# Performance work log

Measured on AMD Instinct MI355X. Metric: run time of the kernel, lower is better.

Reference implementation:

```python
import jax, jax.numpy as jnp
import numpy as np

N_L = 1600   # sample_number_l
N_R = 64     # sample_number_r
F = 512      # num_rgbxyz_feature


def setup_inputs() -> dict:
    key = jax.random.key(0)
    ks = jax.random.split(key, 6)
    soutput_l = jax.random.normal(ks[0], (200000, F), dtype=jnp.float32)
    soutput_r = jax.random.normal(ks[1], (100000, F), dtype=jnp.float32)
    W1 = jax.random.normal(ks[2], (2 * F, 512), dtype=jnp.float32) * 0.02
    b1 = jnp.zeros((512,), dtype=jnp.float32)
    W2 = jax.random.normal(ks[3], (512, 2), dtype=jnp.float32) * 0.02
    b2 = jnp.zeros((2,), dtype=jnp.float32)
    sample_idx_l = jax.random.randint(ks[4], (N_L,), 0, 200000)
    sample_idx_r = jax.random.randint(ks[5], (N_R,), 0, 100000)
    return {
        'soutput_l': soutput_l, 'soutput_r': soutput_r,
        'W1': W1, 'b1': b1, 'W2': W2, 'b2': b2,
        'sample_idx_l': sample_idx_l, 'sample_idx_r': sample_idx_r,
    }


def reference(soutput_l, soutput_r, W1, b1, W2, b2, sample_idx_l, sample_idx_r):
    # Gather sampled per-point features (replaces torch.randint sampling)
    fl = soutput_l[sample_idx_l]          # [N_l, F]
    fr = soutput_r[sample_idx_r]          # [N_r, F]
    n_l, feat = fl.shape
    n_r = fr.shape[0]
    # All-pairs concat: equivalent to the python loop over the 64 right samples,
    # each doing cat((feat_l, feat_r[i].repeat(N_l,1)), dim=1)
    cat = jnp.concatenate([
        jnp.broadcast_to(fl[:, None, :], (n_l, n_r, feat)),
        jnp.broadcast_to(fr[None, :, :], (n_l, n_r, feat)),
    ], axis=-1)                            # [N_l, N_r, 2F]
    # base3DPoseNet: 2-layer MLP (no batch norm), logits over 2 classes
    h = jax.nn.relu(jnp.einsum('lrf,fh->lrh', cat, W1) + b1)   # [N_l, N_r, 512]
    logits = jnp.einsum('lrh,hc->lrc', h, W2) + b2             # [N_l, N_r, 2]
    # softmax over class dim, take P(match) -> correspondence_map[N_l, N_r]
    correspondence_map = jax.nn.softmax(logits, axis=-1)[..., 1]
    return correspondence_map
```

## Files before the change

### kernel.cpp

```cpp
#include <hip/hip_runtime.h>
#include <math.h>

#define FDIM 512
#define NL 1600
#define NR 64

typedef __attribute__((ext_vector_type(8))) short short8;
typedef __attribute__((ext_vector_type(4))) float f32x4;
typedef __attribute__((ext_vector_type(4))) int   int4v;

__device__ __forceinline__ int cvtpk(float lo, float hi) {
    int r;
    asm("v_cvt_pk_bf16_f32 %0, %1, %2" : "=v"(r) : "v"(lo), "v"(hi));
    return r;
}

__global__ __launch_bounds__(64) void k_gemm(
    const float* __restrict__ SL, const float* __restrict__ SR,
    const float* __restrict__ W1, const float* __restrict__ b1,
    const int* __restrict__ idxL, const int* __restrict__ idxR,
    float* __restrict__ A, float* __restrict__ Bm)
{
    const int bm = blockIdx.x;
    const int bn = blockIdx.y;
    const bool isB = bm >= 50;
    const int n0 = bn * 32;
    const int lane = threadIdx.x, row = lane & 15, g = lane >> 4;

    const float* a0p; const float* a1p;
    if (isB) {
        const int rb = (bm - 50) * 32;
        a0p = SR + (long)idxR[rb + row] * FDIM;
        a1p = SR + (long)idxR[rb + 16 + row] * FDIM;
    } else {
        const int mb = bm * 32;
        a0p = SL + (long)idxL[mb + row] * FDIM;
        a1p = SL + (long)idxL[mb + 16 + row] * FDIM;
    }
    const float* w0 = W1 + (isB ? (long)FDIM * FDIM : 0) + (n0 + row);
    const float* w1 = w0 + 16;

    f32x4 acc00 = {}, acc01 = {}, acc10 = {}, acc11 = {};
    float4 a0r[2][2], a1r[2][2];
    float  b0r[2][8], b1r[2][8];

    {
        a0r[0][0] = *(const float4*)(a0p + g * 8);
        a0r[0][1] = *(const float4*)(a0p + g * 8 + 4);
        a1r[0][0] = *(const float4*)(a1p + g * 8);
        a1r[0][1] = *(const float4*)(a1p + g * 8 + 4);
        #pragma unroll
        for (int jj = 0; jj < 8; ++jj) {
            b0r[0][jj] = w0[(long)(g * 8 + jj) * FDIM];
            b1r[0][jj] = w1[(long)(g * 8 + jj) * FDIM];
        }
    }

    #pragma unroll
    for (int kk = 0; kk < 16; ++kk) {
        const int cur = kk & 1, nxt = cur ^ 1;
        if (kk < 15) {
            const int kb = (kk + 1) * 32 + g * 8;
            a0r[nxt][0] = *(const float4*)(a0p + kb);
            a0r[nxt][1] = *(const float4*)(a0p + kb + 4);
            a1r[nxt][0] = *(const float4*)(a1p + kb);
            a1r[nxt][1] = *(const float4*)(a1p + kb + 4);
            #pragma unroll
            for (int jj = 0; jj < 8; ++jj) {
                b0r[nxt][jj] = w0[(long)(kb + jj) * FDIM];
                b1r[nxt][jj] = w1[(long)(kb + jj) * FDIM];
            }
        }
        int4v a0, a1, b0, b1;
        a0.x = cvtpk(a0r[cur][0].x, a0r[cur][0].y);
        a0.y = cvtpk(a0r[cur][0].z, a0r[cur][0].w);
        a0.z = cvtpk(a0r[cur][1].x, a0r[cur][1].y);
        a0.w = cvtpk(a0r[cur][1].z, a0r[cur][1].w);
        a1.x = cvtpk(a1r[cur][0].x, a1r[cur][0].y);
        a1.y = cvtpk(a1r[cur][0].z, a1r[cur][0].w);
        a1.z = cvtpk(a1r[cur][1].x, a1r[cur][1].y);
        a1.w = cvtpk(a1r[cur][1].z, a1r[cur][1].w);
        b0.x = cvtpk(b0r[cur][0], b0r[cur][1]);
        b0.y = cvtpk(b0r[cur][2], b0r[cur][3]);
        b0.z = cvtpk(b0r[cur][4], b0r[cur][5]);
        b0.w = cvtpk(b0r[cur][6], b0r[cur][7]);
        b1.x = cvtpk(b1r[cur][0], b1r[cur][1]);
        b1.y = cvtpk(b1r[cur][2], b1r[cur][3]);
        b1.z = cvtpk(b1r[cur][4], b1r[cur][5]);
        b1.w = cvtpk(b1r[cur][6], b1r[cur][7]);
        const short8 A0 = *(const short8*)&a0, A1 = *(const short8*)&a1;
        const short8 B0 = *(const short8*)&b0, B1 = *(const short8*)&b1;
        acc00 = __builtin_amdgcn_mfma_f32_16x16x32_bf16(A0, B0, acc00, 0, 0, 0);
        acc01 = __builtin_amdgcn_mfma_f32_16x16x32_bf16(A0, B1, acc01, 0, 0, 0);
        acc10 = __builtin_amdgcn_mfma_f32_16x16x32_bf16(A1, B0, acc10, 0, 0, 0);
        acc11 = __builtin_amdgcn_mfma_f32_16x16x32_bf16(A1, B1, acc11, 0, 0, 0);
    }

    #pragma unroll
    for (int r = 0; r < 4; ++r) {
        const int na = n0 + row, nb = n0 + 16 + row;
        const int mr0 = g * 4 + r, mr1 = 16 + g * 4 + r;
        if (isB) {
            const int rb = (bm - 50) * 32;
            const float ba = b1[na], bb = b1[nb];
            Bm[(long)(rb + mr0) * FDIM + na] = acc00[r] + ba;
            Bm[(long)(rb + mr0) * FDIM + nb] = acc01[r] + bb;
            Bm[(long)(rb + mr1) * FDIM + na] = acc10[r] + ba;
            Bm[(long)(rb + mr1) * FDIM + nb] = acc11[r] + bb;
        } else {
            const int mb = bm * 32;
            A[(long)(mb + mr0) * FDIM + na] = acc00[r];
            A[(long)(mb + mr0) * FDIM + nb] = acc01[r];
            A[(long)(mb + mr1) * FDIM + na] = acc10[r];
            A[(long)(mb + mr1) * FDIM + nb] = acc11[r];
        }
    }
}

__global__ __launch_bounds__(256) void k_pair(
    const float* __restrict__ A, const float* __restrict__ Bm,
    const float* __restrict__ W2, float* __restrict__ Part)
{
    __shared__ float4 Bs[16 * 64];
    __shared__ float wdl[64];
    const int t    = threadIdx.x;
    const int lane = t & 63;
    const int w    = t >> 6;
    const int lt   = blockIdx.x;
    const int kq   = blockIdx.y;

    if (t < 32) {
        float4 v = *(const float4*)(&W2[kq * 128 + 4 * t]);
        wdl[2 * t]     = v.y - v.x;
        wdl[2 * t + 1] = v.w - v.z;
    }
    const float4* Bm4 = (const float4*)Bm;
    #pragma unroll
    for (int i = 0; i < 4; ++i) {
        const int idx = i * 256 + t;
        const int r = idx >> 4, c = idx & 15;
        Bs[c * 64 + (r ^ c)] = Bm4[r * 128 + kq * 16 + c];
    }
    __syncthreads();

    const int lb = lt * 16 + w * 4;
    const float4* A0 = (const float4*)(A + (long)(lb + 0) * FDIM) + kq * 16;
    const float4* A1 = (const float4*)(A + (long)(lb + 1) * FDIM) + kq * 16;
    const float4* A2 = (const float4*)(A + (long)(lb + 2) * FDIM) + kq * 16;
    const float4* A3 = (const float4*)(A + (long)(lb + 3) * FDIM) + kq * 16;
    const float4* W4 = (const float4*)wdl;

    float acc0 = 0.f, acc1 = 0.f, acc2 = 0.f, acc3 = 0.f;
    #pragma unroll
    for (int c = 0; c < 16; ++c) {
        float4 b  = Bs[c * 64 + (lane ^ c)];
        float4 wv = W4[c];
        float4 a0 = A0[c], a1 = A1[c], a2 = A2[c], a3 = A3[c];
        acc0 = fmaf(fmaxf(a0.x + b.x, 0.f), wv.x, acc0);
        acc0 = fmaf(fmaxf(a0.y + b.y, 0.f), wv.y, acc0);
        acc0 = fmaf(fmaxf(a0.z + b.z, 0.f), wv.z, acc0);
        acc0 = fmaf(fmaxf(a0.w + b.w, 0.f), wv.w, acc0);
        acc1 = fmaf(fmaxf(a1.x + b.x, 0.f), wv.x, acc1);
        acc1 = fmaf(fmaxf(a1.y + b.y, 0.f), wv.y, acc1);
        acc1 = fmaf(fmaxf(a1.z + b.z, 0.f), wv.z, acc1);
        acc1 = fmaf(fmaxf(a1.w + b.w, 0.f), wv.w, acc1);
        acc2 = fmaf(fmaxf(a2.x + b.x, 0.f), wv.x, acc2);
        acc2 = fmaf(fmaxf(a2.y + b.y, 0.f), wv.y, acc2);
        acc2 = fmaf(fmaxf(a2.z + b.z, 0.f), wv.z, acc2);
        acc2 = fmaf(fmaxf(a2.w + b.w, 0.f), wv.w, acc2);
        acc3 = fmaf(fmaxf(a3.x + b.x, 0.f), wv.x, acc3);
        acc3 = fmaf(fmaxf(a3.y + b.y, 0.f), wv.y, acc3);
        acc3 = fmaf(fmaxf(a3.z + b.z, 0.f), wv.z, acc3);
        acc3 = fmaf(fmaxf(a3.w + b.w, 0.f), wv.w, acc3);
    }
    float* P = Part + ((long)kq * NL + lb) * NR + lane;
    P[0 * NR] = acc0;
    P[1 * NR] = acc1;
    P[2 * NR] = acc2;
    P[3 * NR] = acc3;
}

__global__ __launch_bounds__(256) void k_final(
    const float* __restrict__ Part, const float* __restrict__ b2,
    float* __restrict__ out)
{
    const int gid = blockIdx.x * 256 + threadIdx.x;
    float s = b2[1] - b2[0];
    #pragma unroll
    for (int q = 0; q < 8; ++q) s += Part[(long)q * NL * NR + gid];
    out[gid] = 1.f / (1.f + expf(-s));
}

extern "C" void kernel_launch(void* const* d_in, const int* in_sizes, int n_in,
                              void* d_out, int out_size, void* d_ws, size_t ws_size,
                              hipStream_t stream) {
    const float* SL  = (const float*)d_in[0];
    const float* SR  = (const float*)d_in[1];
    const float* W1  = (const float*)d_in[2];
    const float* b1  = (const float*)d_in[3];
    const float* W2  = (const float*)d_in[4];
    const float* b2  = (const float*)d_in[5];
    const int*   idxL = (const int*)d_in[6];
    const int*   idxR = (const int*)d_in[7];
    float* out = (float*)d_out;

    float* A    = (float*)d_ws;
    float* Bm   = A + (long)NL * FDIM;
    float* Part = Bm + (long)NR * FDIM;

    k_gemm<<<dim3(52, 16), 64, 0, stream>>>(SL, SR, W1, b1, idxL, idxR, A, Bm);
    k_pair<<<dim3(100, 8), 256, 0, stream>>>(A, Bm, W2, Part);
    k_final<<<(NL * NR) / 256, 256, 0, stream>>>(Part, b2, out);
}
```

Before: 30.01 us.

## Fuse partial-sum reduction and sigmoid into pair kernel with bf16 B tile

The pair kernel now covers the full 512-wide hidden dimension in each block: 8 waves each take a 64-channel slice for 4 left rows. Partial sums are reduced through shared memory, and the sigmoid is applied in the same kernel. This removes the k_final launch and the global Part round trip. To fit the whole B matrix (64x512) in LDS, it is stored as packed bf16, which adds unpack instructions and loses precision on B. Each block now reloads all of B from global memory, and there are only 400 blocks of 512 threads.

```diff
diff --git a/kernel.cpp b/kernel.cpp
--- a/kernel.cpp
+++ b/kernel.cpp
@@ -117,78 +117,89 @@
     }
 }
 
-__global__ __launch_bounds__(256) void k_pair(
+__global__ __launch_bounds__(512) void k_pair(
     const float* __restrict__ A, const float* __restrict__ Bm,
-    const float* __restrict__ W2, float* __restrict__ Part)
+    const float* __restrict__ W2, const float* __restrict__ b2,
+    float* __restrict__ out)
 {
-    __shared__ float4 Bs[16 * 64];
-    __shared__ float wdl[64];
+    __shared__ uint2 Bs[128][64];
+    __shared__ float wdl[FDIM];
     const int t    = threadIdx.x;
+    const int w    = t >> 6;
     const int lane = t & 63;
-    const int w    = t >> 6;
-    const int lt   = blockIdx.x;
-    const int kq   = blockIdx.y;
-
-    if (t < 32) {
-        float4 v = *(const float4*)(&W2[kq * 128 + 4 * t]);
+    const int lb   = blockIdx.x * 4;
+
+    if (t < 256) {
+        float4 v = *(const float4*)(&W2[t * 4]);
         wdl[2 * t]     = v.y - v.x;
         wdl[2 * t + 1] = v.w - v.z;
     }
-    const float4* Bm4 = (const float4*)Bm;
-    #pragma unroll
-    for (int i = 0; i < 4; ++i) {
-        const int idx = i * 256 + t;
-        const int r = idx >> 4, c = idx & 15;
-        Bs[c * 64 + (r ^ c)] = Bm4[r * 128 + kq * 16 + c];
+    const float4* B4 = (const float4*)Bm;
+    #pragma unroll
+    for (int i = 0; i < 16; ++i) {
+        const int g = i * 512 + t;
+        const int r = g >> 7, u = g & 127;
+        float4 v = B4[(long)r * 128 + u];
+        uint2 pk;
+        pk.x = (unsigned)cvtpk(v.x, v.y);
+        pk.y = (unsigned)cvtpk(v.z, v.w);
+        Bs[u][r ^ (u & 15)] = pk;
     }
     __syncthreads();
 
-    const int lb = lt * 16 + w * 4;
-    const float4* A0 = (const float4*)(A + (long)(lb + 0) * FDIM) + kq * 16;
-    const float4* A1 = (const float4*)(A + (long)(lb + 1) * FDIM) + kq * 16;
-    const float4* A2 = (const float4*)(A + (long)(lb + 2) * FDIM) + kq * 16;
-    const float4* A3 = (const float4*)(A + (long)(lb + 3) * FDIM) + kq * 16;
-    const float4* W4 = (const float4*)wdl;
+    const float4* A0 = (const float4*)(A + (long)(lb + 0) * FDIM) + w * 16;
+    const float4* A1 = (const float4*)(A + (long)(lb + 1) * FDIM) + w * 16;
+    const float4* A2 = (const float4*)(A + (long)(lb + 2) * FDIM) + w * 16;
+    const float4* A3 = (const float4*)(A + (long)(lb + 3) * FDIM) + w * 16;
+    const float4* W4 = (const float4*)wdl + w * 16;
 
     float acc0 = 0.f, acc1 = 0.f, acc2 = 0.f, acc3 = 0.f;
     #pragma unroll
     for (int c = 0; c < 16; ++c) {
-        float4 b  = Bs[c * 64 + (lane ^ c)];
+        const int u = w * 16 + c;
+        uint2 pk = Bs[u][lane ^ (u & 15)];
+        float bx = __uint_as_float(pk.x << 16);
+        float by = __uint_as_float(pk.x & 0xffff0000u);
+        float bz = __uint_as_float(pk.y << 16);
+        float bw = __uint_as_float(pk.y & 0xffff0000u);
         float4 wv = W4[c];
         float4 a0 = A0[c], a1 = A1[c], a2 = A2[c], a3 = A3[c];
-        acc0 = fmaf(fmaxf(a0.x + b.x, 0.f), wv.x, acc0);
-        acc0 = fmaf(fmaxf(a0.y + b.y, 0.f), wv.y, acc0);
-        acc0 = fmaf(fmaxf(a0.z + b.z, 0.f), wv.z, acc0);
-        acc0 = fmaf(fmaxf(a0.w + b.w, 0.f), wv.w, acc0);
-        acc1 = fmaf(fmaxf(a1.x + b.x, 0.f), wv.x, acc1);
-        acc1 = fmaf(fmaxf(a1.y + b.y, 0.f), wv.y, acc1);
-        acc1 = fmaf(fmaxf(a1.z + b.z, 0.f), wv.z, acc1);
-        acc1 = fmaf(fmaxf(a1.w + b.w, 0.f), wv.w, acc1);
-        acc2 = fmaf(fmaxf(a2.x + b.x, 0.f), wv.x, acc2);
-        acc2 = fmaf(fmaxf(a2.y + b.y, 0.f), wv.y, acc2);
-        acc2 = fmaf(fmaxf(a2.z + b.z, 0.f), wv.z, acc2);
-        acc2 = fmaf(fmaxf(a2.w + b.w, 0.f), wv.w, acc2);
-        acc3 = fmaf(fmaxf(a3.x + b.x, 0.f), wv.x, acc3);
-        acc3 = fmaf(fmaxf(a3.y + b.y, 0.f), wv.y, acc3);
-        acc3 = fmaf(fmaxf(a3.z + b.z, 0.f), wv.z, acc3);
-        acc3 = fmaf(fmaxf(a3.w + b.w, 0.f), wv.w, acc3);
-    }
-    float* P = Part + ((long)kq * NL + lb) * NR + lane;
-    P[0 * NR] = acc0;
-    P[1 * NR] = acc1;
-    P[2 * NR] = acc2;
-    P[3 * NR] = acc3;
-}
-
-__global__ __launch_bounds__(256) void k_final(
-    const float* __restrict__ Part, const float* __restrict__ b2,
-    float* __restrict__ out)
-{
-    const int gid = blockIdx.x * 256 + threadIdx.x;
-    float s = b2[1] - b2[0];
-    #pragma unroll
-    for (int q = 0; q < 8; ++q) s += Part[(long)q * NL * NR + gid];
-    out[gid] = 1.f / (1.f + expf(-s));
+        acc0 = fmaf(fmaxf(a0.x + bx, 0.f), wv.x, acc0);
+        acc0 = fmaf(fmaxf(a0.y + by, 0.f), wv.y, acc0);
+        acc0 = fmaf(fmaxf(a0.z + bz, 0.f), wv.z, acc0);
+        acc0 = fmaf(fmaxf(a0.w + bw, 0.f), wv.w, acc0);
+        acc1 = fmaf(fmaxf(a1.x + bx, 0.f), wv.x, acc1);
+        acc1 = fmaf(fmaxf(a1.y + by, 0.f), wv.y, acc1);
+        acc1 = fmaf(fmaxf(a1.z + bz, 0.f), wv.z, acc1);
+        acc1 = fmaf(fmaxf(a1.w + bw, 0.f), wv.w, acc1);
+        acc2 = fmaf(fmaxf(a2.x + bx, 0.f), wv.x, acc2);
+        acc2 = fmaf(fmaxf(a2.y + by, 0.f), wv.y, acc2);
+        acc2 = fmaf(fmaxf(a2.z + bz, 0.f), wv.z, acc2);
+        acc2 = fmaf(fmaxf(a2.w + bw, 0.f), wv.w, acc2);
+        acc3 = fmaf(fmaxf(a3.x + bx, 0.f), wv.x, acc3);
+        acc3 = fmaf(fmaxf(a3.y + by, 0.f), wv.y, acc3);
+        acc3 = fmaf(fmaxf(a3.z + bz, 0.f), wv.z, acc3);
+        acc3 = fmaf(fmaxf(a3.w + bw, 0.f), wv.w, acc3);
+    }
+    __syncthreads();
+    float* P = (float*)Bs;
+    {
+        const int base = (w * 4) * 64 + lane;
+        P[base]       = acc0;
+        P[base + 64]  = acc1;
+        P[base + 128] = acc2;
+        P[base + 192] = acc3;
+    }
+    __syncthreads();
+
+    if (t < 256) {
+        const int li = t >> 6, rr = t & 63;
+        float s = b2[1] - b2[0];
+        #pragma unroll
+        for (int q = 0; q < 8; ++q)
+            s += P[(q * 4 + li) * 64 + rr];
+        out[(long)(lb + li) * NR + rr] = 1.f / (1.f + expf(-s));
+    }
 }
 
 extern "C" void kernel_launch(void* const* d_in, const int* in_sizes, int n_in,
@@ -204,11 +215,9 @@
     const int*   idxR = (const int*)d_in[7];
     float* out = (float*)d_out;
 
-    float* A    = (float*)d_ws;
-    float* Bm   = A + (long)NL * FDIM;
-    float* Part = Bm + (long)NR * FDIM;
+    float* A  = (float*)d_ws;
+    float* Bm = A + (long)NL * FDIM;
 
     k_gemm<<<dim3(52, 16), 64, 0, stream>>>(SL, SR, W1, b1, idxL, idxR, A, Bm);
-    k_pair<<<dim3(100, 8), 256, 0, stream>>>(A, Bm, W2, Part);
-    k_final<<<(NL * NR) / 256, 256, 0, stream>>>(Part, b2, out);
-}
+    k_pair<<<NL / 4, 512, 0, stream>>>(A, Bm, W2, b2, out);
+}
```

New measurement: 28.59 us. -4.7%, faster.
